# Optimization experiments

Hardware: AMD Instinct MI355X
Metric: run time of the kernel (lower is better)

## Reference

```python
import jax, jax.numpy as jnp
import numpy as np

B, N, D, H = 4, 1024, 1024, 16
DH = D // H
EPS = 1e-5


def setup_inputs() -> dict:
    key = jax.random.key(0)
    ks = jax.random.split(key, 16)
    s = lambda fan_in: 1.0 / np.sqrt(fan_in)
    inp = {
        'x0': jax.random.normal(ks[0], (B, N, D), jnp.float32),
        'x1': jax.random.normal(ks[1], (B, N, D), jnp.float32),
        # weights stored as [in, out]; y = x @ W + b
        'Wqk': jax.random.uniform(ks[2], (D, D), jnp.float32, -s(D), s(D)),
        'bqk': jax.random.uniform(ks[3], (D,), jnp.float32, -s(D), s(D)),
        'Wv': jax.random.uniform(ks[4], (D, D), jnp.float32, -s(D), s(D)),
        'bv': jax.random.uniform(ks[5], (D,), jnp.float32, -s(D), s(D)),
        'Wo': jax.random.uniform(ks[6], (D, D), jnp.float32, -s(D), s(D)),
        'bo': jax.random.uniform(ks[7], (D,), jnp.float32, -s(D), s(D)),
        'Wf1': jax.random.uniform(ks[8], (2 * D, 2 * D), jnp.float32, -s(2 * D), s(2 * D)),
        'bf1': jax.random.uniform(ks[9], (2 * D,), jnp.float32, -s(2 * D), s(2 * D)),
        'gamma': jnp.ones((2 * D,), jnp.float32),
        'beta': jnp.zeros((2 * D,), jnp.float32),
        'Wf2': jax.random.uniform(ks[10], (2 * D, D), jnp.float32, -s(2 * D), s(2 * D)),
        'bf2': jax.random.uniform(ks[11], (D,), jnp.float32, -s(2 * D), s(2 * D)),
    }
    return inp


def _heads(t):
    # [B, N, D] -> [B, H, N, DH]
    b, n, _ = t.shape
    return t.reshape(b, n, H, DH).transpose(0, 2, 1, 3)


def _merge(t):
    # [B, H, N, DH] -> [B, N, D]
    b, h, n, dh = t.shape
    return t.transpose(0, 2, 1, 3).reshape(b, n, h * dh)


def _ffn(z, Wf1, bf1, gamma, beta, Wf2, bf2):
    h = z @ Wf1 + bf1
    mu = jnp.mean(h, axis=-1, keepdims=True)
    var = jnp.mean((h - mu) ** 2, axis=-1, keepdims=True)
    h = (h - mu) * jax.lax.rsqrt(var + EPS) * gamma + beta
    h = jax.nn.gelu(h, approximate=False)
    return h @ Wf2 + bf2


def reference(x0, x1, Wqk, bqk, Wv, bv, Wo, bo, Wf1, bf1, gamma, beta, Wf2, bf2):
    scale = DH ** (-0.5)
    qk0 = _heads(x0 @ Wqk + bqk) * (scale ** 0.5)
    qk1 = _heads(x1 @ Wqk + bqk) * (scale ** 0.5)
    v0 = _heads(x0 @ Wv + bv)
    v1 = _heads(x1 @ Wv + bv)
    # shared similarity matrix [B, H, N0, N1]
    sim = jnp.einsum('bhid,bhjd->bhij', qk0, qk1)
    attn01 = jax.nn.softmax(sim, axis=-1)            # over N1
    attn10 = jax.nn.softmax(sim, axis=-2)            # over N0 (== softmax(sim^T, -1)^T)
    m0 = jnp.einsum('bhij,bhjd->bhid', attn01, v1)   # [B,H,N0,DH]
    m1 = jnp.einsum('bhji,bhjd->bhid', attn10, v0)   # [B,H,N1,DH]
    m0 = _merge(m0) @ Wo + bo
    m1 = _merge(m1) @ Wo + bo
    y0 = x0 + _ffn(jnp.concatenate([x0, m0], -1), Wf1, bf1, gamma, beta, Wf2, bf2)
    y1 = x1 + _ffn(jnp.concatenate([x1, m1], -1), Wf1, bf1, gamma, beta, Wf2, bf2)
    return (y0, y1)
```

## Files before the change

kernel.cpp:

```cpp
#include <hip/hip_runtime.h>
#include <hip/hip_bf16.h>

typedef unsigned short u16;
typedef unsigned int u32;
typedef __attribute__((ext_vector_type(8))) short bf16x8;
typedef __attribute__((ext_vector_type(4))) float f32x4;
typedef __attribute__((ext_vector_type(16))) float f32x16;

#define DEV __device__ __forceinline__
#define FENCE asm volatile("" ::: "memory")
#define WAITL asm volatile("s_waitcnt lgkmcnt(0)" ::: "memory")
#define BAR __builtin_amdgcn_s_barrier()

static constexpr int Bc = 4, Nc = 1024, Dc = 1024, Hc = 16, Mc = 4096, D2c = 2048;
static constexpr size_t VT_STRIDE = (size_t)4 * 16 * 64 * 1024;

DEV u16 f2bf(float f) {
  u32 u = __builtin_bit_cast(u32, f);
  u = (u + 0x7FFFu + ((u >> 16) & 1u)) >> 16;
  return (u16)u;
}
DEV float bf2f(u16 h) { u32 u = ((u32)h) << 16; return __builtin_bit_cast(float, u); }
DEV void gl_lds16(const void* g, void* l) {
  __builtin_amdgcn_global_load_lds((const __attribute__((address_space(1))) u32*)g,
                                   (__attribute__((address_space(3))) u32*)l, 16, 0, 0);
}
DEV int SW(int r, int c) { return c ^ (r & 7) ^ ((r >> 3) & 3); }

DEV float erf_fast(float x) {
  float ax = __builtin_fabsf(x);
  float t = __builtin_amdgcn_rcpf(__builtin_fmaf(0.3275911f, ax, 1.0f));
  float p = __builtin_fmaf(1.061405429f, t, -1.453152027f);
  p = __builtin_fmaf(p, t, 1.421413741f);
  p = __builtin_fmaf(p, t, -0.284496736f);
  p = __builtin_fmaf(p, t, 0.254829592f);
  p *= t;
  float e = __builtin_amdgcn_exp2f(-1.4426950408889634f * ax * ax);
  float r = __builtin_fmaf(-p, e, 1.0f);
  return __builtin_copysignf(r, x);
}
DEV float gelu_exact(float v) {
  return 0.5f * v * (1.0f + erf_fast(v * 0.70710678118654752f));
}

__global__ __launch_bounds__(256) void k_f32_to_bf16(const float* __restrict__ in,
                                                     u16* __restrict__ out, int n) {
  int i = (blockIdx.x * 256 + threadIdx.x) * 8;
  if (i >= n) return;
  float4 a = *(const float4*)(in + i);
  float4 b = *(const float4*)(in + i + 4);
  union { u16 s[8]; uint4 v; } r;
  r.s[0] = f2bf(a.x); r.s[1] = f2bf(a.y); r.s[2] = f2bf(a.z); r.s[3] = f2bf(a.w);
  r.s[4] = f2bf(b.x); r.s[5] = f2bf(b.y); r.s[6] = f2bf(b.z); r.s[7] = f2bf(b.w);
  *(uint4*)(out + i) = r.v;
}

__global__ __launch_bounds__(256) void k_transpose_f32_bf16(const float* __restrict__ in,
                                                            u16* __restrict__ out, int R, int C) {
  __shared__ float t[64][65];
  int c0 = blockIdx.x * 64, r0 = blockIdx.y * 64;
  int tid = threadIdx.x;
  int rr = tid >> 4, cc4 = (tid & 15) * 4;
  for (int k = 0; k < 4; ++k) {
    int r = rr + k * 16;
    float4 v = *(const float4*)(in + (size_t)(r0 + r) * C + c0 + cc4);
    t[r][cc4 + 0] = v.x; t[r][cc4 + 1] = v.y; t[r][cc4 + 2] = v.z; t[r][cc4 + 3] = v.w;
  }
  __syncthreads();
  int cw = tid >> 4, rr4 = (tid & 15) * 4;
  for (int k = 0; k < 4; ++k) {
    int c = cw + k * 16;
    union { u16 s[4]; uint2 v; } p;
    for (int j = 0; j < 4; ++j) p.s[j] = f2bf(t[rr4 + j][c]);
    *(uint2*)(out + (size_t)(c0 + c) * R + r0 + rr4) = p.v;
  }
}

__global__ __launch_bounds__(256) void k_v_transpose(const u16* __restrict__ qkv,
                                                     u16* __restrict__ vt01) {
  __shared__ __align__(16) u16 t[64][80];
  int z = blockIdx.z;
  const u16* v = qkv + (size_t)z * Mc * 2048 + 1024;
  u16* vt = vt01 + (size_t)z * VT_STRIDE;
  int nt = blockIdx.x;
  int bh = blockIdx.y, b = bh >> 4, h = bh & 15;
  int tid = threadIdx.x;
  for (int it = 0; it < 2; ++it) {
    int u = it * 256 + tid; int r = u >> 3, ch = u & 7;
    uint4 raw = *(const uint4*)(v + ((size_t)b * Nc + nt * 64 + r) * 2048 + h * 64 + ch * 8);
    *(uint4*)&t[r][ch * 8] = raw;
  }
  __syncthreads();
  for (int it = 0; it < 2; ++it) {
    int u = it * 256 + tid; int d = u >> 3, nch = u & 7;
    union { u16 s[8]; uint4 v4; } p;
    for (int j = 0; j < 8; ++j) p.s[j] = t[nch * 8 + j][d];
    *(uint4*)(vt + ((size_t)bh * 64 + d) * Nc + nt * 64 + nch * 8) = p.v4;
  }
}

__global__ __launch_bounds__(512, 1) void k_gemm8(
    const u16* __restrict__ A1, int lda1, const u16* __restrict__ A2, int lda2, int kstile,
    const u16* __restrict__ Bt, const float* __restrict__ bias1, const float* __restrict__ bias2,
    int Nsplit, float scale1, float scale2, u16* __restrict__ out, int ldc, int K, int gx) {
  __shared__ __align__(16) u16 lds[65536];
  int tid = threadIdx.x;
  int w = tid >> 6, l = tid & 63;
  int lo = l & 15, hi = l >> 4;
  int wm2 = w >> 2, wn4 = w & 3;
  int nt = K >> 6, niter = nt >> 1;

  int nwg = gridDim.x;
  int swz = (blockIdx.x & 7) * (nwg >> 3) + (blockIdx.x >> 3);
  int m0 = (swz / gx) * 256, n0 = (swz % gx) * 256;

  auto ldsA = [&](int buf, int h) -> u16* { return lds + ((buf << 1) + h) * 8192; };
  auto ldsB = [&](int buf, int h) -> u16* { return lds + 32768 + ((buf << 1) + h) * 8192; };

  auto stageA = [&](int tile, int h) {
    int tt = tile < nt ? tile : 0;
    const u16* base; int ldx, kof;
    if (tt < kstile) { base = A1; ldx = lda1; kof = tt * 64; }
    else             { base = A2; ldx = lda2; kof = (tt - kstile) * 64; }
    u16* dst = ldsA(tile & 1, h);
    size_t row0 = (size_t)(m0 + h * 128);
#pragma unroll
    for (int i = 0; i < 2; ++i) {
      int e = i * 4096 + tid * 8;
      int r = e >> 6, s = (e >> 3) & 7;
      gl_lds16(base + (row0 + r) * (size_t)ldx + kof + 8 * (s ^ (r & 7)), dst + e);
    }
  };
  auto stageB = [&](int tile, int h) {
    int tt = tile < nt ? tile : 0;
    u16* dst = ldsB(tile & 1, h);
    size_t row0 = (size_t)(n0 + h * 128);
#pragma unroll
    for (int i = 0; i < 2; ++i) {
      int e = i * 4096 + tid * 8;
      int r = e >> 6, s = (e >> 3) & 7;
      gl_lds16(Bt + (row0 + r) * (size_t)K + tt * 64 + 8 * (s ^ (r & 7)), dst + e);
    }
  };
  auto loadA = [&](bf16x8 (&a)[4][2], int buf, int qm) {
    const u16* src = ldsA(buf, qm);
#pragma unroll
    for (int mf = 0; mf < 4; ++mf) {
      int r = wm2 * 64 + mf * 16 + lo;
#pragma unroll
      for (int kk = 0; kk < 2; ++kk)
        a[mf][kk] = *(const bf16x8*)&src[r * 64 + (((kk * 4 + hi) ^ (r & 7)) << 3)];
    }
  };
  auto loadB = [&](bf16x8 (&bq)[2][2], int buf, int qn) {
    const u16* src = ldsB(buf, qn);
#pragma unroll
    for (int nf = 0; nf < 2; ++nf) {
      int r = wn4 * 32 + nf * 16 + lo;
#pragma unroll
      for (int kk = 0; kk < 2; ++kk)
        bq[nf][kk] = *(const bf16x8*)&src[r * 64 + (((kk * 4 + hi) ^ (r & 7)) << 3)];
    }
  };

  f32x4 acc00[4][2] = {}, acc01[4][2] = {}, acc10[4][2] = {}, acc11[4][2] = {};
  bf16x8 a[4][2], b0[2][2], b1[2][2];

  auto mmaQ = [&](f32x4 (&accq)[4][2], bf16x8 (&aa)[4][2], bf16x8 (&bb)[2][2]) {
    __builtin_amdgcn_s_setprio(1);
#pragma unroll
    for (int mf = 0; mf < 4; ++mf)
#pragma unroll
      for (int nf = 0; nf < 2; ++nf)
#pragma unroll
        for (int kk = 0; kk < 2; ++kk)
          accq[mf][nf] = __builtin_amdgcn_mfma_f32_16x16x32_bf16(aa[mf][kk], bb[nf][kk], accq[mf][nf], 0, 0, 0);
    __builtin_amdgcn_s_setprio(0);
  };

  stageA(0, 0); stageB(0, 0); stageA(0, 1); stageB(0, 1);
  stageA(1, 0); stageB(1, 0);
  asm volatile("s_waitcnt vmcnt(4)" ::: "memory");
  BAR;

  for (int it = 0; it < niter; ++it) {
    int t0 = 2 * it;
    loadA(a, 0, 0); loadB(b0, 0, 0);
    stageA(t0 + 1, 1);
    FENCE; BAR; WAITL;
    mmaQ(acc00, a, b0);
    FENCE; BAR;
    loadB(b1, 0, 1);
    stageB(t0 + 1, 1);
    FENCE; BAR; WAITL;
    mmaQ(acc01, a, b1);
    FENCE; BAR;
    loadA(a, 0, 1);
    stageA(t0 + 2, 0);
    FENCE; BAR; WAITL;
    mmaQ(acc10, a, b0);
    FENCE; BAR;
    stageB(t0 + 2, 0);
    asm volatile("s_waitcnt vmcnt(4)" ::: "memory");
    BAR;
    mmaQ(acc11, a, b1);
    FENCE; BAR;
    loadA(a, 1, 0); loadB(b0, 1, 0);
    stageA(t0 + 2, 1);
    FENCE; BAR; WAITL;
    mmaQ(acc00, a, b0);
    FENCE; BAR;
    loadB(b1, 1, 1);
    stageB(t0 + 2, 1);
    FENCE; BAR; WAITL;
    mmaQ(acc01, a, b1);
    FENCE; BAR;
    loadA(a, 1, 1);
    stageA(t0 + 3, 0);
    FENCE; BAR; WAITL;
    mmaQ(acc10, a, b0);
    FENCE; BAR;
    stageB(t0 + 3, 0);
    asm volatile("s_waitcnt vmcnt(4)" ::: "memory");
    BAR;
    mmaQ(acc11, a, b1);
    FENCE; BAR;
  }

  auto epi = [&](f32x4 (&accq)[4][2], int qm, int qn) {
#pragma unroll
    for (int mf = 0; mf < 4; ++mf)
#pragma unroll
      for (int nf = 0; nf < 2; ++nf) {
        int col = n0 + qn * 128 + wn4 * 32 + nf * 16 + lo;
        float bb, sc;
        if (col < Nsplit) { bb = bias1[col]; sc = scale1; }
        else              { bb = bias2[col - Nsplit]; sc = scale2; }
        int row = m0 + qm * 128 + wm2 * 64 + mf * 16 + hi * 4;
#pragma unroll
        for (int i = 0; i < 4; ++i)
          out[(size_t)(row + i) * ldc + col] = f2bf((accq[mf][nf][i] + bb) * sc);
      }
  };
  epi(acc00, 0, 0); epi(acc01, 0, 1); epi(acc10, 1, 0); epi(acc11, 1, 1);
}

template <bool OUT_BF16>
__global__ __launch_bounds__(512, 1) void k_gemm8h(
    const u16* __restrict__ A1, int lda1, const u16* __restrict__ Bt,
    const float* __restrict__ bias,
    const float* __restrict__ resid0, const float* __restrict__ resid1, int Msplit,
    void* __restrict__ out, int ldc, int K, int gx) {
  __shared__ __align__(16) u16 lds[49152];
  int tid = threadIdx.x;
  int w = tid >> 6, l = tid & 63;
  int lo = l & 15, hi = l >> 4;
  int wm2 = w >> 2, wn4 = w & 3;
  int nt = K >> 6, niter = nt >> 1;

  int nwg = gridDim.x;
  int swz = (blockIdx.x & 7) * (nwg >> 3) + (blockIdx.x >> 3);
  int m0 = (swz / gx) * 256, n0 = (swz % gx) * 128;

  auto ldsA = [&](int buf, int h) -> u16* { return lds + ((buf << 1) + h) * 8192; };
  auto ldsB = [&](int buf, int h) -> u16* { return lds + 32768 + ((buf << 1) + h) * 4096; };

  auto stageA = [&](int tile, int h) {
    int tt = tile < nt ? tile : 0;
    u16* dst = ldsA(tile & 1, h);
    size_t row0 = (size_t)(m0 + h * 128);
#pragma unroll
    for (int i = 0; i < 2; ++i) {
      int e = i * 4096 + tid * 8;
      int r = e >> 6, s = (e >> 3) & 7;
      gl_lds16(A1 + (row0 + r) * (size_t)lda1 + tt * 64 + 8 * (s ^ (r & 7)), dst + e);
    }
  };
  auto stageB = [&](int tile, int h) {
    int tt = tile < nt ? tile : 0;
    u16* dst = ldsB(tile & 1, h);
    size_t row0 = (size_t)(n0 + h * 64);
    int e = tid * 8;
    int r = e >> 6, s = (e >> 3) & 7;
    gl_lds16(Bt + (row0 + r) * (size_t)K + tt * 64 + 8 * (s ^ (r & 7)), dst + e);
  };
  auto loadA = [&](bf16x8 (&a)[4][2], int buf, int qm) {
    const u16* src = ldsA(buf, qm);
#pragma unroll
    for (int mf = 0; mf < 4; ++mf) {
      int r = wm2 * 64 + mf * 16 + lo;
#pragma unroll
      for (int kk = 0; kk < 2; ++kk)
        a[mf][kk] = *(const bf16x8*)&src[r * 64 + (((kk * 4 + hi) ^ (r & 7)) << 3)];
    }
  };
  auto loadB = [&](bf16x8 (&bq)[2], int buf, int qn) {
    const u16* src = ldsB(buf, qn);
    int r = wn4 * 16 + lo;
#pragma unroll
    for (int kk = 0; kk < 2; ++kk)
      bq[kk] = *(const bf16x8*)&src[r * 64 + (((kk * 4 + hi) ^ (r & 7)) << 3)];
  };

  f32x4 acc00[4] = {}, acc01[4] = {}, acc10[4] = {}, acc11[4] = {};
  bf16x8 a[4][2], b0[2], b1[2];

  auto mma8 = [&](f32x4 (&accq)[4], bf16x8 (&aa)[4][2], bf16x8 (&bb)[2]) {
    __builtin_amdgcn_s_setprio(1);
#pragma unroll
    for (int mf = 0; mf < 4; ++mf)
#pragma unroll
      for (int kk = 0; kk < 2; ++kk)
        accq[mf] = __builtin_amdgcn_mfma_f32_16x16x32_bf16(aa[mf][kk], bb[kk], accq[mf], 0, 0, 0);
    __builtin_amdgcn_s_setprio(0);
  };

  stageA(0, 0); stageB(0, 0); stageA(0, 1); stageB(0, 1);
  stageA(1, 0); stageB(1, 0);
  asm volatile("s_waitcnt vmcnt(3)" ::: "memory");
  BAR;

  for (int it = 0; it < niter; ++it) {
    int t0 = 2 * it;
    loadA(a, 0, 0); loadB(b0, 0, 0);
    stageA(t0 + 1, 1);
    FENCE; BAR; WAITL;
    mma8(acc00, a, b0);
    FENCE; BAR;
    loadB(b1, 0, 1);
    stageB(t0 + 1, 1);
    FENCE; BAR; WAITL;
    mma8(acc01, a, b1);
    FENCE; BAR;
    loadA(a, 0, 1);
    stageA(t0 + 2, 0);
    FENCE; BAR; WAITL;
    mma8(acc10, a, b0);
    FENCE; BAR;
    stageB(t0 + 2, 0);
    asm volatile("s_waitcnt vmcnt(3)" ::: "memory");
    BAR;
    mma8(acc11, a, b1);
    FENCE; BAR;
    loadA(a, 1, 0); loadB(b0, 1, 0);
    stageA(t0 + 2, 1);
    FENCE; BAR; WAITL;
    mma8(acc00, a, b0);
    FENCE; BAR;
    loadB(b1, 1, 1);
    stageB(t0 + 2, 1);
    FENCE; BAR; WAITL;
    mma8(acc01, a, b1);
    FENCE; BAR;
    loadA(a, 1, 1);
    stageA(t0 + 3, 0);
    FENCE; BAR; WAITL;
    mma8(acc10, a, b0);
    FENCE; BAR;
    stageB(t0 + 3, 0);
    asm volatile("s_waitcnt vmcnt(3)" ::: "memory");
    BAR;
    mma8(acc11, a, b1);
    FENCE; BAR;
  }

  auto epi = [&](f32x4 (&accq)[4], int qm, int qn) {
    int col = n0 + qn * 64 + wn4 * 16 + lo;
    float bb = bias[col];
#pragma unroll
    for (int mf = 0; mf < 4; ++mf) {
      int row = m0 + qm * 128 + wm2 * 64 + mf * 16 + hi * 4;
      const float* rsd = nullptr; int roff = 0;
      if (resid0) { if (row < Msplit) { rsd = resid0; } else { rsd = resid1; roff = Msplit; } }
#pragma unroll
      for (int i = 0; i < 4; ++i) {
        float v = accq[mf][i] + bb;
        if (rsd) v += rsd[(size_t)(row + i - roff) * ldc + col];
        if (OUT_BF16) ((u16*)out)[(size_t)(row + i) * ldc + col] = f2bf(v);
        else          ((float*)out)[(size_t)(row + i) * ldc + col] = v;
      }
    }
  };
  epi(acc00, 0, 0); epi(acc01, 0, 1); epi(acc10, 1, 0); epi(acc11, 1, 1);
}

__global__ __launch_bounds__(512, 2) void k_attn(const u16* __restrict__ qkv,
                                                 const u16* __restrict__ vt01,
                                                 u16* __restrict__ m01) {
  __shared__ __align__(16) u16 q_lds[256 * 64];
  __shared__ __align__(16) u16 k_lds[2][64 * 64];
  __shared__ __align__(16) u16 v_lds[2][64 * 64];
  int z = blockIdx.z;
  const u16* Q  = qkv + (size_t)z * Mc * 2048;
  const u16* Kg = qkv + (size_t)(1 - z) * Mc * 2048;
  const u16* Vt = vt01 + (size_t)(1 - z) * VT_STRIDE;
  u16* Out = m01 + (size_t)z * Mc * Dc;
  int tid = threadIdx.x;
  int w = tid >> 6, l = tid & 63;
  int q31 = l & 31, h = l >> 5;
  int qt = blockIdx.x;
  int bh = blockIdx.y, b = bh >> 4, hd = bh & 15;
  size_t rowQ0 = (size_t)b * Nc + qt * 256;

  {
    int r = tid >> 3, s = tid & 7;
#pragma unroll
    for (int c = 0; c < 4; ++c)
      gl_lds16(Q + (rowQ0 + c * 64 + r) * 2048 + hd * 64 + 8 * SW(r, s),
               &q_lds[(size_t)(c * 512 + tid) * 8]);
    gl_lds16(Kg + ((size_t)b * Nc + r) * 2048 + hd * 64 + 8 * SW(r, s), &k_lds[0][(size_t)tid * 8]);
    gl_lds16(Vt + ((size_t)bh * 64 + r) * Nc + 8 * SW(r, s), &v_lds[0][(size_t)tid * 8]);
  }
  __syncthreads();

  bf16x8 qf[4];
  {
    int row = w * 32 + q31;
#pragma unroll
    for (int dk = 0; dk < 4; ++dk)
      qf[dk] = *(const bf16x8*)&q_lds[row * 64 + (SW(row, dk * 2 + h) << 3)];
  }

  f32x16 o0 = {}, o1 = {};
  float ls = 0.f;
  int cur = 0;

  for (int t = 0; t < Nc / 64; ++t) {
    if (t + 1 < Nc / 64) {
      int r = tid >> 3, s = tid & 7;
      gl_lds16(Kg + ((size_t)b * Nc + (t + 1) * 64 + r) * 2048 + hd * 64 + 8 * SW(r, s),
               &k_lds[cur ^ 1][(size_t)tid * 8]);
      gl_lds16(Vt + ((size_t)bh * 64 + r) * Nc + (t + 1) * 64 + 8 * SW(r, s),
               &v_lds[cur ^ 1][(size_t)tid * 8]);
    }

    f32x16 s0 = {}, s1 = {};
    __builtin_amdgcn_s_setprio(1);
#pragma unroll
    for (int dk = 0; dk < 4; ++dk) {
      int r0 = q31, r1 = 32 + q31;
      bf16x8 k0 = *(const bf16x8*)&k_lds[cur][r0 * 64 + (SW(r0, dk * 2 + h) << 3)];
      bf16x8 k1 = *(const bf16x8*)&k_lds[cur][r1 * 64 + (SW(r1, dk * 2 + h) << 3)];
      s0 = __builtin_amdgcn_mfma_f32_32x32x16_bf16(k0, qf[dk], s0, 0, 0, 0);
      s1 = __builtin_amdgcn_mfma_f32_32x32x16_bf16(k1, qf[dk], s1, 0, 0, 0);
    }
    __builtin_amdgcn_s_setprio(0);

    {
      float c16[16];
#pragma unroll
      for (int i = 0; i < 16; ++i) {
        float p0 = exp2f(s0[i]);
        float p1 = exp2f(s1[i]);
        s0[i] = p0; s1[i] = p1;
        c16[i] = p0 + p1;
      }
#pragma unroll
      for (int st = 8; st >= 1; st >>= 1)
#pragma unroll
        for (int i = 0; i < st; ++i) c16[i] += c16[i + st];
      u32 xa = __builtin_bit_cast(u32, c16[0]), xb = xa;
      asm("v_permlane32_swap_b32 %0, %1" : "+v"(xa), "+v"(xb));
      ls += __builtin_bit_cast(float, xa) + __builtin_bit_cast(float, xb);
    }

    u32 pk0[4][2], pk1[4][2];
#pragma unroll
    for (int a2 = 0; a2 < 4; ++a2)
#pragma unroll
      for (int c2 = 0; c2 < 2; ++c2) {
        asm("v_cvt_pk_bf16_f32 %0, %1, %2" : "=v"(pk0[a2][c2]) : "v"(s0[4 * a2 + 2 * c2]), "v"(s0[4 * a2 + 2 * c2 + 1]));
        asm("v_cvt_pk_bf16_f32 %0, %1, %2" : "=v"(pk1[a2][c2]) : "v"(s1[4 * a2 + 2 * c2]), "v"(s1[4 * a2 + 2 * c2 + 1]));
      }
    bf16x8 pf[4];
#pragma unroll
    for (int ks = 0; ks < 4; ++ks) {
      const int aE = (2 * ks) & 3, aO = (2 * ks + 1) & 3;
      u32 x0, y0, x1, y1;
      if (ks < 2) { x0 = pk0[aE][0]; y0 = pk0[aO][0]; x1 = pk0[aE][1]; y1 = pk0[aO][1]; }
      else        { x0 = pk1[aE][0]; y0 = pk1[aO][0]; x1 = pk1[aE][1]; y1 = pk1[aO][1]; }
      asm("v_permlane32_swap_b32 %0, %1" : "+v"(x0), "+v"(y0));
      asm("v_permlane32_swap_b32 %0, %1" : "+v"(x1), "+v"(y1));
      union { u32 u[4]; bf16x8 v; } fu;
      fu.u[0] = x0; fu.u[1] = x1; fu.u[2] = y0; fu.u[3] = y1;
      pf[ks] = fu.v;
    }

    __builtin_amdgcn_s_setprio(1);
#pragma unroll
    for (int ks = 0; ks < 4; ++ks) {
      int r0 = q31, r1 = 32 + q31;
      bf16x8 v0 = *(const bf16x8*)&v_lds[cur][r0 * 64 + (SW(r0, ks * 2 + h) << 3)];
      bf16x8 v1 = *(const bf16x8*)&v_lds[cur][r1 * 64 + (SW(r1, ks * 2 + h) << 3)];
      o0 = __builtin_amdgcn_mfma_f32_32x32x16_bf16(v0, pf[ks], o0, 0, 0, 0);
      o1 = __builtin_amdgcn_mfma_f32_32x32x16_bf16(v1, pf[ks], o1, 0, 0, 0);
    }
    __builtin_amdgcn_s_setprio(0);

    __syncthreads();
    cur ^= 1;
  }

  float inv = 1.f / ls;
  int q_abs = qt * 256 + w * 32 + q31;
  u16* orow = Out + ((size_t)b * Nc + q_abs) * Dc + hd * 64;
#pragma unroll
  for (int rq = 0; rq < 4; ++rq) {
    union { u16 s[4]; uint2 v; } p0, p1;
#pragma unroll
    for (int c = 0; c < 4; ++c) {
      p0.s[c] = f2bf(o0[4 * rq + c] * inv);
      p1.s[c] = f2bf(o1[4 * rq + c] * inv);
    }
    *(uint2*)(orow + 8 * rq + 4 * h) = p0.v;
    *(uint2*)(orow + 32 + 8 * rq + 4 * h) = p1.v;
  }
}

__global__ __launch_bounds__(256) void k_ln_gelu(u16* __restrict__ hbuf,
                                                 const float* __restrict__ gamma,
                                                 const float* __restrict__ beta) {
  int w = threadIdx.x >> 6, l = threadIdx.x & 63;
  int row = blockIdx.x * 4 + w;
  u16* hp = hbuf + (size_t)row * D2c;

  uint4 raw[4];
#pragma unroll
  for (int i = 0; i < 4; ++i)
    raw[i] = *(const uint4*)(hp + (i * 64 + l) * 8);

  float vals[32];
  float s = 0.f, s2 = 0.f;
#pragma unroll
  for (int i = 0; i < 4; ++i) {
    const u16* rs = (const u16*)&raw[i];
#pragma unroll
    for (int j = 0; j < 8; ++j) {
      float v = bf2f(rs[j]);
      vals[i * 8 + j] = v;
      s += v; s2 += v * v;
    }
  }
#pragma unroll
  for (int off = 1; off < 64; off <<= 1) {
    s += __shfl_xor(s, off);
    s2 += __shfl_xor(s2, off);
  }
  float mu = s * (1.f / D2c);
  float var = s2 * (1.f / D2c) - mu * mu;
  float rstd = rsqrtf(var + 1e-5f);

#pragma unroll
  for (int i = 0; i < 4; ++i) {
    int cbase = (i * 64 + l) * 8;
    float4 g0 = *(const float4*)(gamma + cbase);
    float4 g1 = *(const float4*)(gamma + cbase + 4);
    float4 b0 = *(const float4*)(beta + cbase);
    float4 b1 = *(const float4*)(beta + cbase + 4);
    float g[8] = {g0.x, g0.y, g0.z, g0.w, g1.x, g1.y, g1.z, g1.w};
    float bt[8] = {b0.x, b0.y, b0.z, b0.w, b1.x, b1.y, b1.z, b1.w};
    union { u16 s[8]; uint4 v; } o;
#pragma unroll
    for (int j = 0; j < 8; ++j) {
      float v = (vals[i * 8 + j] - mu) * rstd * g[j] + bt[j];
      o.s[j] = f2bf(gelu_exact(v));
    }
    *(uint4*)(hp + cbase) = o.v;
  }
}

extern "C" void kernel_launch(void* const* d_in, const int* in_sizes, int n_in,
                              void* d_out, int out_size, void* d_ws, size_t ws_size,
                              hipStream_t stream) {
  const float* x0   = (const float*)d_in[0];
  const float* x1   = (const float*)d_in[1];
  const float* Wqk  = (const float*)d_in[2];
  const float* bqk  = (const float*)d_in[3];
  const float* Wv   = (const float*)d_in[4];
  const float* bv   = (const float*)d_in[5];
  const float* Wo   = (const float*)d_in[6];
  const float* bo   = (const float*)d_in[7];
  const float* Wf1  = (const float*)d_in[8];
  const float* bf1  = (const float*)d_in[9];
  const float* gamma= (const float*)d_in[10];
  const float* beta = (const float*)d_in[11];
  const float* Wf2  = (const float*)d_in[12];
  const float* bf2  = (const float*)d_in[13];
  float* y = (float*)d_out;

  char* p = (char*)d_ws;
  auto take = [&](size_t elems) { u16* r = (u16*)p; p += ((elems * 2 + 255) & ~(size_t)255); return r; };
  u16* Wqkvt = take((size_t)2048 * 1024);
  u16* Wot   = take((size_t)1024 * 1024);
  u16* Wf1t  = take((size_t)2048 * 2048);
  u16* Wf2t  = take((size_t)2048 * 1024);
  u16* x01b  = take((size_t)8192 * 1024);
  u16* qkv   = take((size_t)8192 * 2048);
  u16* vt01  = take(2 * VT_STRIDE);
  u16* m01   = take((size_t)8192 * 1024);
  u16* h01 = qkv;
  u16* o01 = vt01;

  dim3 blk(256);
  const float sq = 0.4246608984f;

  k_transpose_f32_bf16<<<dim3(16, 16), blk, 0, stream>>>(Wqk, Wqkvt, 1024, 1024);
  k_transpose_f32_bf16<<<dim3(16, 16), blk, 0, stream>>>(Wv, Wqkvt + (size_t)1024 * 1024, 1024, 1024);
  k_transpose_f32_bf16<<<dim3(16, 16), blk, 0, stream>>>(Wo, Wot, 1024, 1024);
  k_transpose_f32_bf16<<<dim3(32, 32), blk, 0, stream>>>(Wf1, Wf1t, 2048, 2048);
  k_transpose_f32_bf16<<<dim3(16, 32), blk, 0, stream>>>(Wf2, Wf2t, 2048, 1024);
  k_f32_to_bf16<<<dim3(2048), blk, 0, stream>>>(x0, x01b, 4096 * 1024);
  k_f32_to_bf16<<<dim3(2048), blk, 0, stream>>>(x1, x01b + (size_t)4096 * 1024, 4096 * 1024);

  k_gemm8<<<dim3(256), dim3(512), 0, stream>>>(
      x01b, 1024, x01b, 1024, 16, Wqkvt,
      bqk, bv, 1024, sq, 1.f, qkv, 2048, 1024, 8);

  k_v_transpose<<<dim3(16, 64, 2), blk, 0, stream>>>(qkv, vt01);

  k_attn<<<dim3(4, 64, 2), dim3(512), 0, stream>>>(qkv, vt01, m01);

  k_gemm8h<true><<<dim3(256), dim3(512), 0, stream>>>(
      m01, 1024, Wot, bo, nullptr, nullptr, 0, o01, 1024, 1024, 8);

  k_gemm8<<<dim3(256), dim3(512), 0, stream>>>(
      x01b, 1024, o01, 1024, 16, Wf1t,
      bf1, nullptr, 2048, 1.f, 1.f, h01, 2048, 2048, 8);

  k_ln_gelu<<<dim3(2048), blk, 0, stream>>>(h01, gamma, beta);

  k_gemm8h<false><<<dim3(256), dim3(512), 0, stream>>>(
      h01, 2048, Wf2t, bf2, x0, x1, 4096, y, 1024, 2048, 8);
}
```

Before: 285.6 us.

## Deepen GEMM LDS prefetch pipeline to two full k-tiles ahead with finer vmcnt waits

Both bf16 GEMM kernels now prefetch two complete k-tiles (all four A/B half-tiles) in the prologue and reorder the in-loop global-to-LDS stage calls so each half-tile is issued earlier. Per-phase vmcnt waits replace the single coarse wait per half-iteration. The aim is to keep more global loads in flight and hide memory latency behind MFMA work. The risk is that a wrong vmcnt count or buffer reuse ordering could cause a race, and the extra in-flight loads add pressure on the memory queue.

```diff
diff --git a/kernel.cpp b/kernel.cpp
--- a/kernel.cpp
+++ b/kernel.cpp
@@ -11,6 +11,7 @@
 #define FENCE asm volatile("" ::: "memory")
 #define WAITL asm volatile("s_waitcnt lgkmcnt(0)" ::: "memory")
 #define BAR __builtin_amdgcn_s_barrier()
+#define VMC(n) asm volatile("s_waitcnt vmcnt(" #n ")" ::: "memory")
 
 static constexpr int Bc = 4, Nc = 1024, Dc = 1024, Hc = 16, Mc = 4096, D2c = 2048;
 static constexpr size_t VT_STRIDE = (size_t)4 * 16 * 64 * 1024;
@@ -178,53 +179,49 @@
     __builtin_amdgcn_s_setprio(0);
   };
 
-  stageA(0, 0); stageB(0, 0); stageA(0, 1); stageB(0, 1);
-  stageA(1, 0); stageB(1, 0);
-  asm volatile("s_waitcnt vmcnt(4)" ::: "memory");
-  BAR;
+  stageA(0, 0); stageB(0, 0); stageB(0, 1); stageA(0, 1);
+  stageA(1, 0); stageB(1, 0); stageB(1, 1); stageA(1, 1);
+  VMC(12); BAR;
 
   for (int it = 0; it < niter; ++it) {
     int t0 = 2 * it;
     loadA(a, 0, 0); loadB(b0, 0, 0);
-    stageA(t0 + 1, 1);
     FENCE; BAR; WAITL;
     mmaQ(acc00, a, b0);
-    FENCE; BAR;
+    FENCE; VMC(10); BAR;
     loadB(b1, 0, 1);
-    stageB(t0 + 1, 1);
+    stageA(t0 + 2, 0);
     FENCE; BAR; WAITL;
     mmaQ(acc01, a, b1);
-    FENCE; BAR;
+    FENCE; VMC(10); BAR;
     loadA(a, 0, 1);
-    stageA(t0 + 2, 0);
+    stageB(t0 + 2, 0);
     FENCE; BAR; WAITL;
     mmaQ(acc10, a, b0);
     FENCE; BAR;
-    stageB(t0 + 2, 0);
-    asm volatile("s_waitcnt vmcnt(4)" ::: "memory");
-    BAR;
+    stageB(t0 + 2, 1);
+    FENCE; BAR;
     mmaQ(acc11, a, b1);
-    FENCE; BAR;
+    FENCE; VMC(10); BAR;
     loadA(a, 1, 0); loadB(b0, 1, 0);
     stageA(t0 + 2, 1);
     FENCE; BAR; WAITL;
     mmaQ(acc00, a, b0);
-    FENCE; BAR;
+    FENCE; VMC(10); BAR;
     loadB(b1, 1, 1);
-    stageB(t0 + 2, 1);
+    stageA(t0 + 3, 0);
     FENCE; BAR; WAITL;
     mmaQ(acc01, a, b1);
-    FENCE; BAR;
+    FENCE; VMC(10); BAR;
     loadA(a, 1, 1);
-    stageA(t0 + 3, 0);
+    stageB(t0 + 3, 0);
     FENCE; BAR; WAITL;
     mmaQ(acc10, a, b0);
     FENCE; BAR;
-    stageB(t0 + 3, 0);
-    asm volatile("s_waitcnt vmcnt(4)" ::: "memory");
-    BAR;
+    stageB(t0 + 3, 1); stageA(t0 + 3, 1);
+    FENCE; BAR;
     mmaQ(acc11, a, b1);
-    FENCE; BAR;
+    FENCE; VMC(12); BAR;
   }
 
   auto epi = [&](f32x4 (&accq)[4][2], int qm, int qn) {
@@ -315,53 +312,49 @@
     __builtin_amdgcn_s_setprio(0);
   };
 
-  stageA(0, 0); stageB(0, 0); stageA(0, 1); stageB(0, 1);
-  stageA(1, 0); stageB(1, 0);
-  asm volatile("s_waitcnt vmcnt(3)" ::: "memory");
-  BAR;
+  stageA(0, 0); stageB(0, 0); stageB(0, 1); stageA(0, 1);
+  stageA(1, 0); stageB(1, 0); stageB(1, 1); stageA(1, 1);
+  VMC(9); BAR;
 
   for (int it = 0; it < niter; ++it) {
     int t0 = 2 * it;
     loadA(a, 0, 0); loadB(b0, 0, 0);
-    stageA(t0 + 1, 1);
     FENCE; BAR; WAITL;
     mma8(acc00, a, b0);
-    FENCE; BAR;
+    FENCE; VMC(8); BAR;
     loadB(b1, 0, 1);
-    stageB(t0 + 1, 1);
+    stageA(t0 + 2, 0);
     FENCE; BAR; WAITL;
     mma8(acc01, a, b1);
-    FENCE; BAR;
+    FENCE; VMC(8); BAR;
     loadA(a, 0, 1);
-    stageA(t0 + 2, 0);
+    stageB(t0 + 2, 0);
     FENCE; BAR; WAITL;
     mma8(acc10, a, b0);
     FENCE; BAR;
-    stageB(t0 + 2, 0);
-    asm volatile("s_waitcnt vmcnt(3)" ::: "memory");
-    BAR;
+    stageB(t0 + 2, 1);
+    FENCE; BAR;
     mma8(acc11, a, b1);
-    FENCE; BAR;
+    FENCE; VMC(7); BAR;
     loadA(a, 1, 0); loadB(b0, 1, 0);
     stageA(t0 + 2, 1);
     FENCE; BAR; WAITL;
     mma8(acc00, a, b0);
-    FENCE; BAR;
+    FENCE; VMC(8); BAR;
     loadB(b1, 1, 1);
-    stageB(t0 + 2, 1);
+    stageA(t0 + 3, 0);
     FENCE; BAR; WAITL;
     mma8(acc01, a, b1);
-    FENCE; BAR;
+    FENCE; VMC(8); BAR;
     loadA(a, 1, 1);
-    stageA(t0 + 3, 0);
+    stageB(t0 + 3, 0);
     FENCE; BAR; WAITL;
     mma8(acc10, a, b0);
     FENCE; BAR;
-    stageB(t0 + 3, 0);
-    asm volatile("s_waitcnt vmcnt(3)" ::: "memory");
-    BAR;
+    stageB(t0 + 3, 1); stageA(t0 + 3, 1);
+    FENCE; BAR;
     mma8(acc11, a, b1);
-    FENCE; BAR;
+    FENCE; VMC(9); BAR;
   }
 
   auto epi = [&](f32x4 (&accq)[4], int qm, int qn) {
```

New measurement: 285.2 us. Within noise of the previous version (-0.1%).
